# Performance work log

Hardware: AMD Instinct MI355X
Metric: run time of the kernel (lower is better)

The kernel has to match this reference:

```python
import jax, jax.numpy as jnp
import numpy as np

D = 1024
LN_EPS = 1e-5


def setup_inputs() -> dict:
    key = jax.random.key(0)
    k1, k2 = jax.random.split(key)
    L, B = 2048, 8
    x = jax.random.normal(k1, (L, B, D), dtype=jnp.float32)
    c = jnp.zeros((B, D), dtype=jnp.float32)
    W = jax.random.normal(k2, (3 * D, D), dtype=jnp.float32) * (1.0 / np.sqrt(D))
    # bias: forget-gate slice [D:2D] initialized to 1.5, rest zero (matches _init_bias)
    b = jnp.zeros((3 * D,), dtype=jnp.float32).at[D:2 * D].set(1.5)
    ln_g = jnp.ones((D,), dtype=jnp.float32)
    ln_b = jnp.zeros((D,), dtype=jnp.float32)
    return {"x": x, "c": c, "W": W, "b": b, "ln_g": ln_g, "ln_b": ln_b}


def _layernorm(x, g, b):
    mu = jnp.mean(x, axis=-1, keepdims=True)
    var = jnp.mean(jnp.square(x - mu), axis=-1, keepdims=True)
    return (x - mu) * jax.lax.rsqrt(var + LN_EPS) * g + b


def _sru_forward(x, c, W, b, ln_g, ln_b):
    residual = x
    x_norm = _layernorm(x, ln_g, ln_b)          # [L, B, D]
    ufr = jnp.einsum('lbd,ed->lbe', x_norm, W) + b  # [L, B, 3D]
    u, f, r = jnp.split(ufr, 3, axis=-1)
    f_gate = jax.nn.sigmoid(f)
    r_gate = jax.nn.sigmoid(r)
    u_tanh = jnp.tanh(u)

    def step(c_prev, inputs):
        f_t, u_t = inputs
        c_t = f_t * c_prev + (1.0 - f_t) * u_t
        return c_t, c_t

    last_c, c_stack = jax.lax.scan(step, c, (f_gate, u_tanh))  # [L, B, D]
    hs = r_gate * jnp.tanh(c_stack) + (1.0 - r_gate) * x_norm
    return residual + hs, last_c


def reference(x, c, W, b, ln_g, ln_b):
    return _sru_forward(x, c, W, b, ln_g, ln_b)
```

## Files before the change

kernel.cpp:

```cpp
#include <hip/hip_runtime.h>

#define L_DIM 2048
#define B_DIM 8
#define DD    1024
#define M_DIM 16384
#define N_DIM 3072
#define K_DIM 1024
#define CH    8192
#define CH8   1024
#define NSEG  128
#define LSEG  16
#define LN_EPS 1e-5f

typedef __attribute__((ext_vector_type(8))) short bf16x8;
typedef __attribute__((ext_vector_type(8))) unsigned short u16x8;
typedef __attribute__((ext_vector_type(4))) float f32x4;

__device__ __forceinline__ unsigned short f2bf(float f){
  unsigned u = __float_as_uint(f);
  u += 0x7fffu + ((u >> 16) & 1u);
  return (unsigned short)(u >> 16);
}
__device__ __forceinline__ float bf2f(unsigned short h){
  return __uint_as_float(((unsigned)h) << 16);
}
__device__ __forceinline__ float fsigmoid(float z){ return 1.0f/(1.0f + __expf(-z)); }
__device__ __forceinline__ float ftanh(float z){ return 1.0f - 2.0f/(1.0f + __expf(2.0f*z)); }

__global__ __launch_bounds__(256) void ln_kernel(const float* __restrict__ x,
                                                 const float* __restrict__ g,
                                                 const float* __restrict__ bta,
                                                 unsigned short* __restrict__ xn)
{
  int tid  = threadIdx.x;
  int wave = tid >> 6, lane = tid & 63;
  int row  = blockIdx.x * 4 + wave;
  const float4* xr = (const float4*)(x + (size_t)row * DD);
  float4 v[4];
  #pragma unroll
  for (int k = 0; k < 4; k++) v[k] = xr[lane + k * 64];
  float s = 0.f, sq = 0.f;
  #pragma unroll
  for (int k = 0; k < 4; k++) {
    s  += v[k].x + v[k].y + v[k].z + v[k].w;
    sq += v[k].x*v[k].x + v[k].y*v[k].y + v[k].z*v[k].z + v[k].w*v[k].w;
  }
  #pragma unroll
  for (int off = 32; off > 0; off >>= 1) {
    s  += __shfl_down(s,  off, 64);
    sq += __shfl_down(sq, off, 64);
  }
  s  = __shfl(s,  0, 64);
  sq = __shfl(sq, 0, 64);
  float mean = s * (1.0f / DD);
  float var  = sq * (1.0f / DD) - mean * mean;
  float rstd = rsqrtf(var + LN_EPS);
  ushort4* xo = (ushort4*)(xn + (size_t)row * DD);
  #pragma unroll
  for (int k = 0; k < 4; k++) {
    float4 gg = ((const float4*)g)[lane + k * 64];
    float4 bb = ((const float4*)bta)[lane + k * 64];
    ushort4 o;
    o.x = f2bf((v[k].x - mean) * rstd * gg.x + bb.x);
    o.y = f2bf((v[k].y - mean) * rstd * gg.y + bb.y);
    o.z = f2bf((v[k].z - mean) * rstd * gg.z + bb.z);
    o.w = f2bf((v[k].w - mean) * rstd * gg.w + bb.w);
    xo[lane + k * 64] = o;
  }
}

__global__ __launch_bounds__(256) void wconv_kernel(const float* __restrict__ W,
                                                    unsigned short* __restrict__ wb)
{
  int gid = blockIdx.x * 256 + threadIdx.x;
  float4 v = ((const float4*)W)[gid];
  ushort4 o;
  o.x = f2bf(v.x); o.y = f2bf(v.y); o.z = f2bf(v.z); o.w = f2bf(v.w);
  ((ushort4*)wb)[gid] = o;
}

#define BM 256
#define BN 256
#define BK 64
#define NT 16
#define LDPE 264

#define GLDS16(gp, lp) __builtin_amdgcn_global_load_lds( \
    (const __attribute__((address_space(1))) void*)(gp), \
    (__attribute__((address_space(3))) void*)(lp), 16, 0, 0)

#define SBAR()   __builtin_amdgcn_s_barrier()
#define SCHED0() __builtin_amdgcn_sched_barrier(0)
#define WAIT_LGKM0() do { asm volatile("s_waitcnt lgkmcnt(0)" ::: "memory"); SCHED0(); } while(0)
#define WAIT_VM(N)   do { asm volatile("s_waitcnt vmcnt(" #N ")" ::: "memory"); SCHED0(); } while(0)

__global__ __launch_bounds__(512, 2) void gemm_gates(const unsigned short* __restrict__ Ag,
                                                     const unsigned short* __restrict__ Bg,
                                                     const float* __restrict__ bias,
                                                     unsigned short* __restrict__ u_t,
                                                     unsigned short* __restrict__ f_g,
                                                     unsigned short* __restrict__ r_g)
{
  __shared__ unsigned short smem[65536];
  const int tid  = threadIdx.x;
  const int wave = tid >> 6, lane = tid & 63;
  const int wm = wave >> 2, wn = wave & 3;
  const int r8 = lane >> 3;
  const int sch = (lane & 7) ^ r8;
  const int fm = lane & 15, quad = lane >> 4, f7 = fm & 7;
  const int bm0 = blockIdx.x * BM, bn0 = blockIdx.y * BN;

  f32x4 zero = {0.f, 0.f, 0.f, 0.f};
  f32x4 acc[8][4];
  #pragma unroll
  for (int i = 0; i < 8; i++)
    #pragma unroll
    for (int j = 0; j < 4; j++) acc[i][j] = zero;

#define STAGE_A(BUF, T, HALF) do { \
  GLDS16(Ag + (size_t)(bm0 + (HALF)*128 + wave*16 + 0 + r8) * K_DIM + ((T)*BK + sch*8), \
         &smem[(BUF)*16384 + ((HALF)*128 + wave*16 + 0) * 64]); \
  GLDS16(Ag + (size_t)(bm0 + (HALF)*128 + wave*16 + 8 + r8) * K_DIM + ((T)*BK + sch*8), \
         &smem[(BUF)*16384 + ((HALF)*128 + wave*16 + 8) * 64]); \
} while(0)

#define STAGE_B(BUF, T, HALF) do { \
  GLDS16(Bg + (size_t)(bn0 + (HALF)*128 + wave*16 + 0 + r8) * K_DIM + ((T)*BK + sch*8), \
         &smem[32768 + (BUF)*16384 + ((HALF)*128 + wave*16 + 0) * 64]); \
  GLDS16(Bg + (size_t)(bn0 + (HALF)*128 + wave*16 + 8 + r8) * K_DIM + ((T)*BK + sch*8), \
         &smem[32768 + (BUF)*16384 + ((HALF)*128 + wave*16 + 8) * 64]); \
} while(0)

#define LOAD_A(MH) do { \
  _Pragma("unroll") for (int i_ = 0; i_ < 4; ++i_) \
  _Pragma("unroll") for (int kk_ = 0; kk_ < 2; ++kk_) \
    a_[i_][kk_] = *(const bf16x8*)&smem[cb*16384 + \
        (wm*128 + (MH)*64 + i_*16 + fm)*64 + (((kk_*4 + quad) ^ f7))*8]; \
} while(0)

#define LOAD_B(NH, DEST) do { \
  _Pragma("unroll") for (int j_ = 0; j_ < 2; ++j_) \
  _Pragma("unroll") for (int kk_ = 0; kk_ < 2; ++kk_) \
    DEST[j_][kk_] = *(const bf16x8*)&smem[32768 + cb*16384 + \
        (wn*64 + (NH)*32 + j_*16 + fm)*64 + (((kk_*4 + quad) ^ f7))*8]; \
} while(0)

#define QMFMA(MH, NH, BREG) do { \
  _Pragma("unroll") for (int i_ = 0; i_ < 4; ++i_) \
  _Pragma("unroll") for (int j_ = 0; j_ < 2; ++j_) \
  _Pragma("unroll") for (int kk_ = 0; kk_ < 2; ++kk_) \
    acc[(MH)*4 + i_][(NH)*2 + j_] = __builtin_amdgcn_mfma_f32_16x16x32_bf16( \
        a_[i_][kk_], BREG[j_][kk_], acc[(MH)*4 + i_][(NH)*2 + j_], 0, 0, 0); \
} while(0)

  bf16x8 a_[4][2], b0_[2][2], b1_[2][2];

  STAGE_A(0, 0, 0); STAGE_A(0, 0, 1);
  STAGE_B(0, 0, 0); STAGE_B(0, 0, 1);
  STAGE_B(1, 1, 0); STAGE_B(1, 1, 1);
  WAIT_VM(4);
  SBAR();

  for (int t = 0; t < NT; ++t) {
    const int cb = t & 1, nb = cb ^ 1;
    LOAD_A(0);
    LOAD_B(0, b0_);
    if (t + 1 < NT) STAGE_A(nb, t + 1, 0);
    SCHED0(); SBAR();
    WAIT_LGKM0();
    __builtin_amdgcn_s_setprio(1);
    QMFMA(0, 0, b0_);
    __builtin_amdgcn_s_setprio(0);
    SBAR();
    LOAD_B(1, b1_);
    if (t + 1 < NT) STAGE_A(nb, t + 1, 1);
    SCHED0(); SBAR();
    WAIT_LGKM0();
    __builtin_amdgcn_s_setprio(1);
    QMFMA(0, 1, b1_);
    __builtin_amdgcn_s_setprio(0);
    SBAR();
    LOAD_A(1);
    if (t + 2 < NT) STAGE_B(cb, t + 2, 0);
    SCHED0(); SBAR();
    WAIT_LGKM0();
    __builtin_amdgcn_s_setprio(1);
    QMFMA(1, 1, b1_);
    __builtin_amdgcn_s_setprio(0);
    SBAR();
    if (t + 2 < NT) STAGE_B(cb, t + 2, 1);
    SCHED0();
    if (t < NT - 2)       WAIT_VM(4);
    else if (t == NT - 2) WAIT_VM(0);
    SBAR();
    __builtin_amdgcn_s_setprio(1);
    QMFMA(1, 0, b0_);
    __builtin_amdgcn_s_setprio(0);
    SBAR();
  }
  __syncthreads();

  const int slice = bn0 >> 10;
  const int nd0   = bn0 & 1023;
  unsigned short* dst = (slice == 0) ? u_t : ((slice == 1) ? f_g : r_g);

  #pragma unroll
  for (int h = 0; h < 2; ++h) {
    if (wm == h) {
      #pragma unroll
      for (int ni = 0; ni < 4; ++ni) {
        int lcol = wn * 64 + ni * 16 + fm;
        float bia = bias[bn0 + lcol];
        #pragma unroll
        for (int mi = 0; mi < 8; ++mi) {
          #pragma unroll
          for (int reg = 0; reg < 4; ++reg) {
            int lrow = mi * 16 + quad * 4 + reg;
            float v = acc[mi][ni][reg] + bia;
            float act = (slice == 0) ? ftanh(v) : fsigmoid(v);
            smem[lrow * LDPE + lcol] = f2bf(act);
          }
        }
      }
    }
    __syncthreads();
    #pragma unroll
    for (int it = 0; it < 8; ++it) {
      int row = it * 16 + (tid >> 5);
      int cc  = (tid & 31) * 8;
      u16x8 v = *(const u16x8*)&smem[row * LDPE + cc];
      *(u16x8*)(dst + (size_t)(bm0 + h * 128 + row) * DD + nd0 + cc) = v;
    }
    __syncthreads();
  }
}

__global__ __launch_bounds__(256) void scan_pass1(const unsigned short* __restrict__ f_g,
                                                  const unsigned short* __restrict__ u_t,
                                                  unsigned short* __restrict__ P,
                                                  unsigned short* __restrict__ E)
{
  int vc8 = blockIdx.x * 256 + threadIdx.x;
  int seg = blockIdx.y;
  const u16x8* f8 = (const u16x8*)f_g;
  const u16x8* u8 = (const u16x8*)u_t;
  size_t g = (size_t)(seg * LSEG) * CH8 + vc8;
  float p[8], e[8];
  #pragma unroll
  for (int k = 0; k < 8; k++) { p[k] = 1.f; e[k] = 0.f; }
  #pragma unroll 4
  for (int i = 0; i < LSEG; i++) {
    u16x8 ff = f8[g];
    u16x8 uu = u8[g];
    #pragma unroll
    for (int k = 0; k < 8; k++) {
      float fv = bf2f(ff[k]);
      e[k] = fv * e[k] + (1.f - fv) * bf2f(uu[k]);
      p[k] *= fv;
    }
    g += CH8;
  }
  u16x8 pv, ev;
  #pragma unroll
  for (int k = 0; k < 8; k++) { pv[k] = f2bf(p[k]); ev[k] = f2bf(e[k]); }
  ((u16x8*)P)[(size_t)seg * CH8 + vc8] = pv;
  ((u16x8*)E)[(size_t)seg * CH8 + vc8] = ev;
}

__global__ __launch_bounds__(128) void scan_pass2(const unsigned short* __restrict__ P,
                                                  const unsigned short* __restrict__ E,
                                                  const float* __restrict__ c0,
                                                  float* __restrict__ Cini,
                                                  float* __restrict__ lastc)
{
  int ch = blockIdx.x * 128 + threadIdx.x;
  float c = c0[ch];
  #pragma unroll 8
  for (int s = 0; s < NSEG; s++) {
    Cini[(size_t)s * CH + ch] = c;
    c = bf2f(P[(size_t)s * CH + ch]) * c + bf2f(E[(size_t)s * CH + ch]);
  }
  lastc[ch] = c;
}

__global__ __launch_bounds__(256) void scan_pass3(const unsigned short* __restrict__ f_g,
                                                  const unsigned short* __restrict__ u_t,
                                                  const unsigned short* __restrict__ r_g,
                                                  const float* __restrict__ x,
                                                  const unsigned short* __restrict__ xn,
                                                  const float* __restrict__ Cini,
                                                  float* __restrict__ out)
{
  int vc8 = blockIdx.x * 256 + threadIdx.x;
  int seg = blockIdx.y;
  const u16x8* f8 = (const u16x8*)f_g;
  const u16x8* u8 = (const u16x8*)u_t;
  const u16x8* r8 = (const u16x8*)r_g;
  const u16x8* n8 = (const u16x8*)xn;
  const float4* x4 = (const float4*)x;
  float4* o4 = (float4*)out;
  float c[8];
  {
    const float4* C4 = (const float4*)Cini;
    size_t ci = (size_t)seg * (CH / 4) + (size_t)vc8 * 2;
    float4 ca = C4[ci], cb = C4[ci + 1];
    c[0]=ca.x; c[1]=ca.y; c[2]=ca.z; c[3]=ca.w;
    c[4]=cb.x; c[5]=cb.y; c[6]=cb.z; c[7]=cb.w;
  }
  size_t g = (size_t)(seg * LSEG) * CH8 + vc8;
  #pragma unroll 2
  for (int i = 0; i < LSEG; i++) {
    u16x8 ff = f8[g];
    u16x8 uu = u8[g];
    u16x8 rr = r8[g];
    u16x8 nn = n8[g];
    size_t xi = g * 2;
    float4 xa = x4[xi], xb = x4[xi + 1];
    float ov[8];
    #pragma unroll
    for (int k = 0; k < 8; k++) {
      float fv = bf2f(ff[k]);
      c[k] = fv * c[k] + (1.f - fv) * bf2f(uu[k]);
      float rv = bf2f(rr[k]);
      ov[k] = rv * ftanh(c[k]) + (1.f - rv) * bf2f(nn[k]);
    }
    o4[xi]     = (float4){xa.x + ov[0], xa.y + ov[1], xa.z + ov[2], xa.w + ov[3]};
    o4[xi + 1] = (float4){xb.x + ov[4], xb.y + ov[5], xb.z + ov[6], xb.w + ov[7]};
    g += CH8;
  }
}

extern "C" void kernel_launch(void* const* d_in, const int* in_sizes, int n_in,
                              void* d_out, int out_size, void* d_ws, size_t ws_size,
                              hipStream_t stream) {
  const float* x    = (const float*)d_in[0];
  const float* c0   = (const float*)d_in[1];
  const float* W    = (const float*)d_in[2];
  const float* bias = (const float*)d_in[3];
  const float* ln_g = (const float*)d_in[4];
  const float* ln_b = (const float*)d_in[5];
  float* out = (float*)d_out;

  char* ws = (char*)d_ws;
  unsigned short* xn  = (unsigned short*)(ws);
  unsigned short* wb  = (unsigned short*)(ws + 33554432ULL);
  unsigned short* u_t = (unsigned short*)(ws + 39845888ULL);
  unsigned short* f_g = (unsigned short*)(ws + 73400320ULL);
  unsigned short* r_g = (unsigned short*)(ws + 106954752ULL);
  unsigned short* Pseg = (unsigned short*)(ws + 33554432ULL);
  unsigned short* Eseg = (unsigned short*)(ws + 35651584ULL);
  float* Cini = (float*)(ws + 140509184ULL);

  ln_kernel   <<<M_DIM / 4, 256, 0, stream>>>(x, ln_g, ln_b, xn);
  wconv_kernel<<<N_DIM, 256, 0, stream>>>(W, wb);
  gemm_gates  <<<dim3(M_DIM / BM, N_DIM / BN), 512, 0, stream>>>(xn, wb, bias, u_t, f_g, r_g);
  scan_pass1  <<<dim3(CH8 / 256, NSEG), 256, 0, stream>>>(f_g, u_t, Pseg, Eseg);
  scan_pass2  <<<CH / 128, 128, 0, stream>>>(Pseg, Eseg, c0, Cini, out + (size_t)M_DIM * DD);
  scan_pass3  <<<dim3(CH8 / 256, NSEG), 256, 0, stream>>>(f_g, u_t, r_g, x, xn, Cini, out);
}
```

Before: 235.6 us.

## Prefetch A half-tile earlier and use inline ds_read with immediate offsets

Replaces the computed LDS loads with inline-asm ds_read_b128 that use precomputed base addresses and immediate offsets, cutting per-load address arithmetic. It reschedules global-to-LDS staging so the first half of the next A tile is issued one iteration earlier, alongside the second B half, and moves the vmcnt wait after the last MFMA group to overlap more memory latency. It also fully unrolls the k-loop. The deeper prefetch raises outstanding loads and ties correctness to the buffer-reuse ordering being right, while the unroll grows code size.

```diff
diff --git a/kernel.cpp b/kernel.cpp
--- a/kernel.cpp
+++ b/kernel.cpp
@@ -94,6 +94,9 @@
 #define WAIT_LGKM0() do { asm volatile("s_waitcnt lgkmcnt(0)" ::: "memory"); SCHED0(); } while(0)
 #define WAIT_VM(N)   do { asm volatile("s_waitcnt vmcnt(" #N ")" ::: "memory"); SCHED0(); } while(0)
 
+#define DSR(dst, addr, IMM) \
+  asm volatile("ds_read_b128 %0, %1 offset:" #IMM : "=v"(dst) : "v"(addr))
+
 __global__ __launch_bounds__(512, 2) void gemm_gates(const unsigned short* __restrict__ Ag,
                                                      const unsigned short* __restrict__ Bg,
                                                      const float* __restrict__ bias,
@@ -131,18 +134,18 @@
          &smem[32768 + (BUF)*16384 + ((HALF)*128 + wave*16 + 8) * 64]); \
 } while(0)
 
-#define LOAD_A(MH) do { \
-  _Pragma("unroll") for (int i_ = 0; i_ < 4; ++i_) \
-  _Pragma("unroll") for (int kk_ = 0; kk_ < 2; ++kk_) \
-    a_[i_][kk_] = *(const bf16x8*)&smem[cb*16384 + \
-        (wm*128 + (MH)*64 + i_*16 + fm)*64 + (((kk_*4 + quad) ^ f7))*8]; \
-} while(0)
-
-#define LOAD_B(NH, DEST) do { \
-  _Pragma("unroll") for (int j_ = 0; j_ < 2; ++j_) \
-  _Pragma("unroll") for (int kk_ = 0; kk_ < 2; ++kk_) \
-    DEST[j_][kk_] = *(const bf16x8*)&smem[32768 + cb*16384 + \
-        (wn*64 + (NH)*32 + j_*16 + fm)*64 + (((kk_*4 + quad) ^ f7))*8]; \
+#define RD_A(CBB, MH) do { \
+  unsigned a0 = (CBB) + aBase + (MH)*8192; unsigned a1 = a0 ^ 64u; \
+  DSR(a_[0][0], a0, 0);    DSR(a_[0][1], a1, 0); \
+  DSR(a_[1][0], a0, 2048); DSR(a_[1][1], a1, 2048); \
+  DSR(a_[2][0], a0, 4096); DSR(a_[2][1], a1, 4096); \
+  DSR(a_[3][0], a0, 6144); DSR(a_[3][1], a1, 6144); \
+} while(0)
+
+#define RD_B(CBB, NH, D) do { \
+  unsigned b0a = (CBB) + bBase + (NH)*4096; unsigned b1a = b0a ^ 64u; \
+  DSR(D[0][0], b0a, 0);    DSR(D[0][1], b1a, 0); \
+  DSR(D[1][0], b0a, 2048); DSR(D[1][1], b1a, 2048); \
 } while(0)
 
 #define QMFMA(MH, NH, BREG) do { \
@@ -154,33 +157,38 @@
 } while(0)
 
   bf16x8 a_[4][2], b0_[2][2], b1_[2][2];
+  const unsigned slot0 = (unsigned)((quad ^ f7) << 4);
+  const unsigned aBase = (unsigned)((wm * 128 + fm) * 128) + slot0;
+  const unsigned bBase = 65536u + (unsigned)((wn * 64 + fm) * 128) + slot0;
 
   STAGE_A(0, 0, 0); STAGE_A(0, 0, 1);
   STAGE_B(0, 0, 0); STAGE_B(0, 0, 1);
   STAGE_B(1, 1, 0); STAGE_B(1, 1, 1);
-  WAIT_VM(4);
+  STAGE_A(1, 1, 0);
+  WAIT_VM(6);
   SBAR();
 
+  #pragma unroll
   for (int t = 0; t < NT; ++t) {
     const int cb = t & 1, nb = cb ^ 1;
-    LOAD_A(0);
-    LOAD_B(0, b0_);
-    if (t + 1 < NT) STAGE_A(nb, t + 1, 0);
+    const unsigned cbB = (unsigned)(cb * 32768);
+    RD_A(cbB, 0);
+    RD_B(cbB, 0, b0_);
+    if (t + 1 < NT) STAGE_A(nb, t + 1, 1);
     SCHED0(); SBAR();
     WAIT_LGKM0();
     __builtin_amdgcn_s_setprio(1);
     QMFMA(0, 0, b0_);
     __builtin_amdgcn_s_setprio(0);
     SBAR();
-    LOAD_B(1, b1_);
-    if (t + 1 < NT) STAGE_A(nb, t + 1, 1);
+    RD_B(cbB, 1, b1_);
     SCHED0(); SBAR();
     WAIT_LGKM0();
     __builtin_amdgcn_s_setprio(1);
     QMFMA(0, 1, b1_);
     __builtin_amdgcn_s_setprio(0);
     SBAR();
-    LOAD_A(1);
+    RD_A(cbB, 1);
     if (t + 2 < NT) STAGE_B(cb, t + 2, 0);
     SCHED0(); SBAR();
     WAIT_LGKM0();
@@ -188,14 +196,13 @@
     QMFMA(1, 1, b1_);
     __builtin_amdgcn_s_setprio(0);
     SBAR();
-    if (t + 2 < NT) STAGE_B(cb, t + 2, 1);
+    if (t + 2 < NT) { STAGE_B(cb, t + 2, 1); STAGE_A(cb, t + 2, 0); }
     SCHED0();
-    if (t < NT - 2)       WAIT_VM(4);
-    else if (t == NT - 2) WAIT_VM(0);
-    SBAR();
     __builtin_amdgcn_s_setprio(1);
     QMFMA(1, 0, b0_);
     __builtin_amdgcn_s_setprio(0);
+    if (t < NT - 2)       WAIT_VM(6);
+    else if (t == NT - 2) WAIT_VM(0);
     SBAR();
   }
   __syncthreads();
```

New measurement: 237.8 us. Within noise of the previous version (+0.9%).
